# Kernel tuning notes

Measured on AMD Instinct MI355X. Metric: run time of the kernel, lower is better.

Reference implementation:

```python
import jax, jax.numpy as jnp
import numpy as np

V = 10000   # vocab_size
L = 12      # n_layer
H = 12      # n_head
C = 768     # n_embd
TE = 64     # t_embd
WTE = C - TE
BS = 1024   # block_size
B, T = 4, 1024
D = C // H
EPS = 1e-5


def setup_inputs() -> dict:
    key = jax.random.key(0)
    ks = jax.random.split(key, 12)
    s = 0.02
    def n(k, shape, extra=1.0):
        return jax.random.normal(k, shape, jnp.float32) * (s * extra)
    resid_scale = 1.0 / np.sqrt(2 * L)  # c_proj init std scaling from _init_weights loop
    return {
        'idx': jax.random.randint(ks[0], (B, T), 0, V),
        'ts': jax.random.uniform(ks[1], (B, T), jnp.float32) * 100.0,
        'wte': n(ks[2], (V, WTE)),
        'basis_freq': jnp.asarray(1.0 / 10 ** np.linspace(0, 9, TE), jnp.float32),
        'phase': jnp.zeros((TE,), jnp.float32),
        'wpe': n(ks[3], (BS, C)),
        'ln1_w': jnp.ones((L, C), jnp.float32), 'ln1_b': jnp.zeros((L, C), jnp.float32),
        'qkv_w': n(ks[4], (L, 3 * C, C)), 'qkv_b': jnp.zeros((L, 3 * C), jnp.float32),
        'proj_w': n(ks[5], (L, C, C), resid_scale), 'proj_b': jnp.zeros((L, C), jnp.float32),
        'ln2_w': jnp.ones((L, C), jnp.float32), 'ln2_b': jnp.zeros((L, C), jnp.float32),
        'fc_w': n(ks[6], (L, 4 * C, C)), 'fc_b': jnp.zeros((L, 4 * C), jnp.float32),
        'fc2_w': n(ks[7], (L, C, 4 * C), resid_scale), 'fc2_b': jnp.zeros((L, C), jnp.float32),
        'lnf_w': jnp.ones((C,), jnp.float32), 'lnf_b': jnp.zeros((C,), jnp.float32),
        'lm_w': n(ks[8], (V, C)),
        'tp_w': n(ks[9], (1, C)),
    }


def _ln(x, w, b):
    mu = jnp.mean(x, -1, keepdims=True)
    var = jnp.mean((x - mu) ** 2, -1, keepdims=True)
    return (x - mu) * jax.lax.rsqrt(var + EPS) * w + b


def reference(idx, ts, wte, basis_freq, phase, wpe, ln1_w, ln1_b, qkv_w, qkv_b,
              proj_w, proj_b, ln2_w, ln2_b, fc_w, fc_b, fc2_w, fc2_b,
              lnf_w, lnf_b, lm_w, tp_w):
    Bv, Tv = idx.shape
    tok = wte[idx]                                      # [B,T,C-TE]
    tim = jnp.cos(ts[..., None] * basis_freq + phase)   # TimeEncode -> [B,T,TE]
    x = jnp.concatenate([tok, tim], axis=-1) + wpe[:Tv]
    mask = jnp.tril(jnp.ones((Tv, Tv), bool))
    scale = 1.0 / np.sqrt(D)

    def block(x, p):
        l1w, l1b, qw, qb, pw, pb, l2w, l2b, fw, fb, f2w, f2b = p
        h = _ln(x, l1w, l1b)
        qkv = h @ qw.T + qb                              # [B,T,3C]
        q, k, v = jnp.split(qkv, 3, axis=-1)
        def heads(z):
            return z.reshape(Bv, Tv, H, D).transpose(0, 2, 1, 3)  # [B,H,T,D]
        q, k, v = heads(q), heads(k), heads(v)
        att = jnp.einsum('bhtd,bhsd->bhts', q, k) * scale
        att = jnp.where(mask, att, -jnp.inf)             # causal masked_fill
        att = jax.nn.softmax(att, axis=-1)
        y = jnp.einsum('bhts,bhsd->bhtd', att, v)
        y = y.transpose(0, 2, 1, 3).reshape(Bv, Tv, C)
        x = x + (y @ pw.T + pb)
        h2 = _ln(x, l2w, l2b)
        m = jax.nn.gelu(h2 @ fw.T + fb, approximate=False)  # torch nn.GELU default is exact
        x = x + (m @ f2w.T + f2b)
        return x, None

    x, _ = jax.lax.scan(block, x, (ln1_w, ln1_b, qkv_w, qkv_b, proj_w, proj_b,
                                   ln2_w, ln2_b, fc_w, fc_b, fc2_w, fc2_b))
    x = _ln(x, lnf_w, lnf_b)
    logits = x @ lm_w.T          # [B,T,V]
    tpred = x @ tp_w.T           # [B,T,1]
    return logits, tpred
```

## Files before the change

### kernel.cpp

```cpp
#include <hip/hip_runtime.h>
#include <hip/hip_bf16.h>
#include <math.h>

#define Bb   4
#define Tt   1024
#define Cc   768
#define Hh   12
#define Dd   64
#define Ll   12
#define Vv   10000
#define WTEe 704
#define MTOT 4096

#define QSCALE 0.18033688f

typedef __bf16 bf16x8 __attribute__((ext_vector_type(8)));
typedef float  f32x4  __attribute__((ext_vector_type(4)));
typedef unsigned short u16;

typedef const __attribute__((address_space(1))) void* gptr_t;
typedef __attribute__((address_space(3))) void* lptr_t;

__device__ inline void gload16(const void* g, void* l) {
    __builtin_amdgcn_global_load_lds((gptr_t)g, (lptr_t)l, 16, 0, 0);
}

__device__ inline u16 f2bf(float f) {
    unsigned int u = __float_as_uint(f);
    return (u16)((u + 0x7fffu + ((u >> 16) & 1u)) >> 16);
}
__device__ inline float bf2f(u16 u) { return __uint_as_float(((unsigned)u) << 16); }

__device__ inline float gelu_f(float v) {
    float t = v * (0.797884561f + 0.0356774081f * v * v);
    float e = __expf(2.f * t);
    float th = 1.f - 2.f / (e + 1.f);
    return 0.5f * v * (1.f + th);
}

#if __has_builtin(__builtin_amdgcn_exp2f)
__device__ inline float fast_exp2(float x) { return __builtin_amdgcn_exp2f(x); }
#else
__device__ inline float fast_exp2(float x) { return exp2f(x); }
#endif

#define WAITVM(N)  asm volatile("s_waitcnt vmcnt(" #N ")" ::: "memory")
#define WAITLGKM0() asm volatile("s_waitcnt lgkmcnt(0)" ::: "memory")
#define SCHEDB()   __builtin_amdgcn_sched_barrier(0)
#define SBAR()     __builtin_amdgcn_s_barrier()

__global__ __launch_bounds__(256)
void convert_pack(const float* __restrict__ in, u16* __restrict__ out,
                  int nk8, int K, int rowmod, int scaleLim)
{
    int i = blockIdx.x * 256 + threadIdx.x;
    if (i >= nk8) return;
    int row = (i << 3) / K;
    int col = (i << 3) % K;
    float s = 1.f;
    if (rowmod && (row % rowmod) < scaleLim) s = QSCALE;
    float4 v0 = ((const float4*)in)[2 * i];
    float4 v1 = ((const float4*)in)[2 * i + 1];
    uint4 o;
    o.x = (unsigned)f2bf(v0.x * s) | ((unsigned)f2bf(v0.y * s) << 16);
    o.y = (unsigned)f2bf(v0.z * s) | ((unsigned)f2bf(v0.w * s) << 16);
    o.z = (unsigned)f2bf(v1.x * s) | ((unsigned)f2bf(v1.y * s) << 16);
    o.w = (unsigned)f2bf(v1.z * s) | ((unsigned)f2bf(v1.w * s) << 16);
    int tile = row >> 4, kt = col >> 5;
    int l = (row & 15) | (((col >> 3) & 3) << 4);
    size_t off = (((size_t)tile * (K >> 5) + kt) << 9) + l * 8;
    *(uint4*)(out + off) = o;
}

__global__ __launch_bounds__(256)
void scale_qkvb(const float* __restrict__ in, float* __restrict__ out, int n)
{
    int i = blockIdx.x * 256 + threadIdx.x;
    if (i >= n) return;
    int col = i % (3 * Cc);
    out[i] = in[i] * (col < Cc ? QSCALE : 1.f);
}

__global__ __launch_bounds__(256)
void embed_kernel(const int* __restrict__ idx, const float* __restrict__ ts,
                  const float* __restrict__ wte, const float* __restrict__ freq,
                  const float* __restrict__ ph, const float* __restrict__ wpe,
                  float* __restrict__ x)
{
    const int bt  = blockIdx.x;
    const int t   = bt & (Tt - 1);
    const int tok = idx[bt];
    const float tv = ts[bt];
#pragma unroll
    for (int j = 0; j < 3; ++j) {
        int c = threadIdx.x + (j << 8);
        float val;
        if (c < WTEe) val = wte[(size_t)tok * WTEe + c];
        else {
            int e = c - WTEe;
            val = cosf(tv * freq[e] + ph[e]);
        }
        x[(size_t)bt * Cc + c] = val + wpe[(size_t)t * Cc + c];
    }
}

__global__ __launch_bounds__(256)
void ln_pack16(const float* __restrict__ x, const float* __restrict__ wt,
               const float* __restrict__ bs, u16* __restrict__ out)
{
    __shared__ float ps[256], ps2[256];
    const int tid  = threadIdx.x;
    const int tile = blockIdx.x;
    const int r0   = tile << 4;
    const int row  = tid & 15;
    const int g    = (tid >> 4) & 3;
    const int kt0  = tid >> 6;

    const float* xr = x + (size_t)(r0 + row) * Cc;
    float4 va[6], vb[6];
    float s = 0.f, s2 = 0.f;
#pragma unroll
    for (int it = 0; it < 6; ++it) {
        int col = (kt0 + 4 * it) * 32 + g * 8;
        va[it] = *(const float4*)(xr + col);
        vb[it] = *(const float4*)(xr + col + 4);
        s  += va[it].x + va[it].y + va[it].z + va[it].w
            + vb[it].x + vb[it].y + vb[it].z + vb[it].w;
        s2 += va[it].x * va[it].x + va[it].y * va[it].y
            + va[it].z * va[it].z + va[it].w * va[it].w
            + vb[it].x * vb[it].x + vb[it].y * vb[it].y
            + vb[it].z * vb[it].z + vb[it].w * vb[it].w;
    }
    ps[tid] = s;
    ps2[tid] = s2;
    __syncthreads();

    float st = 0.f, st2 = 0.f;
#pragma unroll
    for (int j = 0; j < 16; ++j) {
        st  += ps[row + 16 * j];
        st2 += ps2[row + 16 * j];
    }
    float mu = st * (1.f / 768.f);
    float var = st2 * (1.f / 768.f) - mu * mu;
    float rs = rsqrtf(var + 1e-5f);

    u16* ob = out + ((size_t)tile * 24 << 9);
    const int l = tid & 63;
#pragma unroll
    for (int it = 0; it < 6; ++it) {
        int kt  = kt0 + 4 * it;
        int col = kt * 32 + g * 8;
        ushort o[8];
        o[0] = f2bf((va[it].x - mu) * rs * wt[col]     + bs[col]);
        o[1] = f2bf((va[it].y - mu) * rs * wt[col + 1] + bs[col + 1]);
        o[2] = f2bf((va[it].z - mu) * rs * wt[col + 2] + bs[col + 2]);
        o[3] = f2bf((va[it].w - mu) * rs * wt[col + 3] + bs[col + 3]);
        o[4] = f2bf((vb[it].x - mu) * rs * wt[col + 4] + bs[col + 4]);
        o[5] = f2bf((vb[it].y - mu) * rs * wt[col + 5] + bs[col + 5]);
        o[6] = f2bf((vb[it].z - mu) * rs * wt[col + 6] + bs[col + 6]);
        o[7] = f2bf((vb[it].w - mu) * rs * wt[col + 7] + bs[col + 7]);
        *(uint4*)(ob + ((size_t)kt << 9) + l * 8) = *(uint4*)o;
    }
}

__device__ inline void st_out(float* p, size_t o, float v) { p[o] = v; }
__device__ inline void st_out(u16*   p, size_t o, float v) { p[o] = f2bf(v); }

template<int EPI, int APK, typename OutT>
__global__ __launch_bounds__(256)
void gemm_bf16(const u16* __restrict__ A, const u16* __restrict__ Wp,
               const float* __restrict__ bias, const float* __restrict__ resid,
               OutT* __restrict__ out, u16* __restrict__ vt, int N, int K)
{
    __shared__ uint4 AF[3][8][64];
    __shared__ uint4 BF[3][8][64];
    const int tid  = threadIdx.x;
    const int lane = tid & 63;
    const int w    = tid >> 6;
    const int wr   = w >> 1, wc = w & 1;
    const int lq   = lane & 15, g = lane >> 4;
    const int m0   = blockIdx.x * 128, n0 = blockIdx.y * 128;
    const int KB   = K >> 5;

    const u16 *ap0, *ap1;
    if (APK) {
        ap0 = A + ((((size_t)(m0 >> 4) + 2 * w) * KB) << 9) + lane * 8;
        ap1 = ap0 + ((size_t)KB << 9);
    } else {
        ap0 = A + (size_t)(m0 + (2 * w) * 16 + lq) * K + g * 8;
        ap1 = ap0 + (size_t)16 * K;
    }

    int tn0 = (n0 >> 4) + 2 * w, tn1 = tn0 + 1;
    const int tmax = (N >> 4) - 1;
    tn0 = tn0 < tmax ? tn0 : tmax;
    tn1 = tn1 < tmax ? tn1 : tmax;
    const u16* bq0 = Wp + (((size_t)tn0 * KB) << 9) + lane * 8;
    const u16* bq1 = Wp + (((size_t)tn1 * KB) << 9) + lane * 8;

    f32x4 acc[4][4] = {};
    const int nk = KB;

#define GSTAGE(s, sl) do {                                               \
        if (APK) {                                                       \
            gload16(ap0 + ((size_t)(s) << 9), &AF[sl][2 * w][lane]);     \
            gload16(ap1 + ((size_t)(s) << 9), &AF[sl][2 * w + 1][lane]); \
        } else {                                                         \
            gload16(ap0 + ((s) << 5), &AF[sl][2 * w][lane]);             \
            gload16(ap1 + ((s) << 5), &AF[sl][2 * w + 1][lane]);         \
        }                                                                \
        gload16(bq0 + ((size_t)(s) << 9), &BF[sl][2 * w][lane]);         \
        gload16(bq1 + ((size_t)(s) << 9), &BF[sl][2 * w + 1][lane]); } while (0)

    GSTAGE(0, 0);
    GSTAGE(1, 1);
    WAITVM(4);
    SCHEDB();
    SBAR();
    SCHEDB();

    int sl = 0;
    for (int t = 0; t < nk; ++t) {
        int sl2 = sl + 2; if (sl2 >= 3) sl2 -= 3;
        if (t + 2 < nk) GSTAGE(t + 2, sl2);

        bf16x8 af[4], bfr[4];
#pragma unroll
        for (int mi = 0; mi < 4; ++mi)
            af[mi] = __builtin_bit_cast(bf16x8, AF[sl][wr * 4 + mi][lane]);
#pragma unroll
        for (int ni = 0; ni < 4; ++ni)
            bfr[ni] = __builtin_bit_cast(bf16x8, BF[sl][wc * 4 + ni][lane]);
        __builtin_amdgcn_s_setprio(1);
#pragma unroll
        for (int mi = 0; mi < 4; ++mi)
#pragma unroll
            for (int ni = 0; ni < 4; ++ni)
                acc[mi][ni] = __builtin_amdgcn_mfma_f32_16x16x32_bf16(
                    af[mi], bfr[ni], acc[mi][ni], 0, 0, 0);
        __builtin_amdgcn_s_setprio(0);

        if (t + 2 < nk) { WAITVM(4); }
        else           { WAITVM(0); }
        SCHEDB();
        SBAR();
        SCHEDB();
        sl = (sl + 1 == 3) ? 0 : sl + 1;
    }
#undef GSTAGE

    if (EPI == 3 && n0 >= 1536) {
#pragma unroll
        for (int mi = 0; mi < 4; ++mi)
#pragma unroll
            for (int ni = 0; ni < 4; ++ni) {
                int col = n0 + wc * 64 + ni * 16 + lq;
                int c2  = col - 1536;
                int hh  = c2 >> 6, dd = c2 & 63;
                int row = m0 + wr * 64 + mi * 16 + g * 4;
                int bb  = row >> 10, tr = row & 1023;
                float bv = bias[col];
                ushort4 o;
                o.x = f2bf(acc[mi][ni][0] + bv);
                o.y = f2bf(acc[mi][ni][1] + bv);
                o.z = f2bf(acc[mi][ni][2] + bv);
                o.w = f2bf(acc[mi][ni][3] + bv);
                *(ushort4*)&vt[(((size_t)bb * Hh + hh) * Dd + dd) * Tt + tr] = o;
            }
        return;
    }

#pragma unroll
    for (int mi = 0; mi < 4; ++mi)
#pragma unroll
        for (int ni = 0; ni < 4; ++ni) {
            int col = n0 + wc * 64 + ni * 16 + lq;
            if (col >= N) continue;
            int row = m0 + wr * 64 + mi * 16 + g * 4;
            float bv = bias ? bias[col] : 0.f;
#pragma unroll
            for (int q = 0; q < 4; ++q) {
                float v = acc[mi][ni][q] + bv;
                size_t o = (size_t)(row + q) * N + col;
                if (EPI == 1) v += resid[o];
                if (EPI == 2) v = gelu_f(v);
                st_out(out, o, v);
            }
        }
}

__global__ __launch_bounds__(256)
void gemm_n64(const u16* __restrict__ A, const u16* __restrict__ Wp,
              const float* __restrict__ bias, const float* __restrict__ resid,
              float* __restrict__ out, int N, int K)
{
    __shared__ uint4 AF[2][8][64];
    __shared__ uint4 BF[2][16][64];
    const int tid  = threadIdx.x;
    const int lane = tid & 63;
    const int w    = tid >> 6;
    const int wr   = w & 1, wc = w >> 1;
    const int lq   = lane & 15, g = lane >> 4;
    const int m0   = blockIdx.x * 64, n0 = blockIdx.y * 128;
    const int KB   = K >> 5;
    const int nk   = K >> 6;

    const u16* ap = A + (size_t)(m0 + w * 16 + lq) * K + g * 8;
    int tn0 = (n0 >> 4) + 2 * w, tn1 = tn0 + 1;
    const int tmax = (N >> 4) - 1;
    tn0 = tn0 < tmax ? tn0 : tmax;
    tn1 = tn1 < tmax ? tn1 : tmax;
    const u16* bq0 = Wp + (((size_t)tn0 * KB) << 9) + lane * 8;
    const u16* bq1 = Wp + (((size_t)tn1 * KB) << 9) + lane * 8;

    f32x4 acc[2][4] = {};

#define GSTAGE(t, bi) do {                                                 \
        gload16(ap + ((t) << 6),      &AF[bi][2 * w][lane]);               \
        gload16(ap + ((t) << 6) + 32, &AF[bi][2 * w + 1][lane]);           \
        gload16(bq0 + ((size_t)(2 * (t)) << 9),     &BF[bi][4 * w][lane]); \
        gload16(bq0 + ((size_t)(2 * (t) + 1) << 9), &BF[bi][4 * w + 1][lane]); \
        gload16(bq1 + ((size_t)(2 * (t)) << 9),     &BF[bi][4 * w + 2][lane]); \
        gload16(bq1 + ((size_t)(2 * (t) + 1) << 9), &BF[bi][4 * w + 3][lane]); } while (0)

    GSTAGE(0, 0);
    WAITVM(0);
    SCHEDB();
    SBAR();
    SCHEDB();

    for (int t = 0; t < nk; ++t) {
        const int buf = t & 1;
        if (t + 1 < nk) GSTAGE(t + 1, buf ^ 1);

#pragma unroll
        for (int s = 0; s < 2; ++s) {
            bf16x8 a0 = __builtin_bit_cast(bf16x8, AF[buf][(wr * 2) * 2 + s][lane]);
            bf16x8 a1 = __builtin_bit_cast(bf16x8, AF[buf][(wr * 2 + 1) * 2 + s][lane]);
            bf16x8 bb[4];
#pragma unroll
            for (int ni = 0; ni < 4; ++ni)
                bb[ni] = __builtin_bit_cast(bf16x8, BF[buf][(wc * 4 + ni) * 2 + s][lane]);
            __builtin_amdgcn_s_setprio(1);
#pragma unroll
            for (int ni = 0; ni < 4; ++ni) {
                acc[0][ni] = __builtin_amdgcn_mfma_f32_16x16x32_bf16(
                    bb[ni], a0, acc[0][ni], 0, 0, 0);
                acc[1][ni] = __builtin_amdgcn_mfma_f32_16x16x32_bf16(
                    bb[ni], a1, acc[1][ni], 0, 0, 0);
            }
            __builtin_amdgcn_s_setprio(0);
        }

        WAITVM(0);
        SCHEDB();
        SBAR();
        SCHEDB();
    }
#undef GSTAGE

#pragma unroll
    for (int mi = 0; mi < 2; ++mi)
#pragma unroll
        for (int ni = 0; ni < 4; ++ni) {
            int m = m0 + (wr * 2 + mi) * 16 + lq;
            int n = n0 + wc * 64 + ni * 16 + (g << 2);
            float4 bv = *(const float4*)&bias[n];
            size_t o = (size_t)m * N + n;
            float4 rv = *(const float4*)&resid[o];
            float4 v;
            v.x = acc[mi][ni][0] + bv.x + rv.x;
            v.y = acc[mi][ni][1] + bv.y + rv.y;
            v.z = acc[mi][ni][2] + bv.z + rv.z;
            v.w = acc[mi][ni][3] + bv.w + rv.w;
            *(float4*)&out[o] = v;
        }
}

__global__ __launch_bounds__(512, 2)
void gemm8p(const u16* __restrict__ Apk, const u16* __restrict__ Wp,
            float* __restrict__ out, int N, int K)
{
    __shared__ uint4 AF[2][16][2][64];
    __shared__ uint4 BF[2][16][2][64];
    const int tid  = threadIdx.x;
    const int lane = tid & 63;
    const int w    = tid >> 6;
    const int wr   = w >> 2, wc = w & 3;
    const int lq   = lane & 15, g = lane >> 4;
    const int m0   = blockIdx.x * 256, n0 = blockIdx.y * 256;
    const int KB   = K >> 5;

    const u16* aq0 = Apk + ((((size_t)(m0 >> 4) + 2 * w) * KB) << 9) + lane * 8;
    const u16* aq1 = aq0 + ((size_t)KB << 9);

    int tn0 = (n0 >> 4) + 2 * w, tn1 = tn0 + 1;
    const int tmax = (N >> 4) - 1;
    tn0 = tn0 < tmax ? tn0 : tmax;
    tn1 = tn1 < tmax ? tn1 : tmax;
    const u16* bq0 = Wp + (((size_t)tn0 * KB) << 9) + lane * 8;
    const u16* bq1 = Wp + (((size_t)tn1 * KB) << 9) + lane * 8;

    f32x4 acc[8][4] = {};
    const int nt = K >> 6;

    gload16(aq0,       &AF[0][2 * w][0][lane]);
    gload16(aq1,       &AF[0][2 * w + 1][0][lane]);
    gload16(bq0,       &BF[0][2 * w][0][lane]);
    gload16(bq1,       &BF[0][2 * w + 1][0][lane]);
    gload16(aq0 + 512, &AF[0][2 * w][1][lane]);
    gload16(aq1 + 512, &AF[0][2 * w + 1][1][lane]);
    gload16(bq0 + 512, &BF[0][2 * w][1][lane]);
    gload16(bq1 + 512, &BF[0][2 * w + 1][1][lane]);
    WAITVM(0);
    SCHEDB();
    SBAR();

    int buf = 0;
    for (int t = 0; t < nt; ++t) {
        const bool more = (t + 1 < nt);
        const size_t bb0 = (size_t)(2 * (t + 1)) << 9;
        bf16x8 a0[4], a1[4], b0[4];

#pragma unroll
        for (int i = 0; i < 4; ++i)
            a0[i] = __builtin_bit_cast(bf16x8, AF[buf][wr * 8 + i][0][lane]);
#pragma unroll
        for (int i = 0; i < 4; ++i)
            b0[i] = __builtin_bit_cast(bf16x8, BF[buf][wc * 4 + i][0][lane]);
        if (more) {
            gload16(aq0 + bb0, &AF[buf ^ 1][2 * w][0][lane]);
            gload16(aq1 + bb0, &AF[buf ^ 1][2 * w + 1][0][lane]);
        }
        SCHEDB();
        SBAR();
        WAITLGKM0();
        SCHEDB();
        __builtin_amdgcn_s_setprio(1);
#pragma unroll
        for (int mi = 0; mi < 4; ++mi)
#pragma unroll
            for (int ni = 0; ni < 4; ++ni)
                acc[mi][ni] = __builtin_amdgcn_mfma_f32_16x16x32_bf16(
                    b0[ni], a0[mi], acc[mi][ni], 0, 0, 0);
        __builtin_amdgcn_s_setprio(0);
        SBAR();

#pragma unroll
        for (int i = 0; i < 4; ++i)
            a1[i] = __builtin_bit_cast(bf16x8, AF[buf][wr * 8 + 4 + i][0][lane]);
        if (more) {
            gload16(bq0 + bb0, &BF[buf ^ 1][2 * w][0][lane]);
            gload16(bq1 + bb0, &BF[buf ^ 1][2 * w + 1][0][lane]);
        }
        SCHEDB();
        SBAR();
        WAITLGKM0();
        SCHEDB();
        __builtin_amdgcn_s_setprio(1);
#pragma unroll
        for (int mi = 0; mi < 4; ++mi)
#pragma unroll
            for (int ni = 0; ni < 4; ++ni)
                acc[4 + mi][ni] = __builtin_amdgcn_mfma_f32_16x16x32_bf16(
                    b0[ni], a1[mi], acc[4 + mi][ni], 0, 0, 0);
        __builtin_amdgcn_s_setprio(0);
        if (more) { WAITVM(4); } else { WAITVM(0); }
        SCHEDB();
        SBAR();

#pragma unroll
        for (int i = 0; i < 4; ++i)
            a0[i] = __builtin_bit_cast(bf16x8, AF[buf][wr * 8 + i][1][lane]);
#pragma unroll
        for (int i = 0; i < 4; ++i)
            b0[i] = __builtin_bit_cast(bf16x8, BF[buf][wc * 4 + i][1][lane]);
        if (more) {
            gload16(aq0 + bb0 + 512, &AF[buf ^ 1][2 * w][1][lane]);
            gload16(aq1 + bb0 + 512, &AF[buf ^ 1][2 * w + 1][1][lane]);
        }
        SCHEDB();
        SBAR();
        WAITLGKM0();
        SCHEDB();
        __builtin_amdgcn_s_setprio(1);
#pragma unroll
        for (int mi = 0; mi < 4; ++mi)
#pragma unroll
            for (int ni = 0; ni < 4; ++ni)
                acc[mi][ni] = __builtin_amdgcn_mfma_f32_16x16x32_bf16(
                    b0[ni], a0[mi], acc[mi][ni], 0, 0, 0);
        __builtin_amdgcn_s_setprio(0);
        SBAR();

#pragma unroll
        for (int i = 0; i < 4; ++i)
            a1[i] = __builtin_bit_cast(bf16x8, AF[buf][wr * 8 + 4 + i][1][lane]);
        if (more) {
            gload16(bq0 + bb0 + 512, &BF[buf ^ 1][2 * w][1][lane]);
            gload16(bq1 + bb0 + 512, &BF[buf ^ 1][2 * w + 1][1][lane]);
        }
        SCHEDB();
        SBAR();
        WAITLGKM0();
        SCHEDB();
        __builtin_amdgcn_s_setprio(1);
#pragma unroll
        for (int mi = 0; mi < 4; ++mi)
#pragma unroll
            for (int ni = 0; ni < 4; ++ni)
                acc[4 + mi][ni] = __builtin_amdgcn_mfma_f32_16x16x32_bf16(
                    b0[ni], a1[mi], acc[4 + mi][ni], 0, 0, 0);
        __builtin_amdgcn_s_setprio(0);
        if (more) { WAITVM(4); } else { WAITVM(0); }
        SCHEDB();
        SBAR();

        buf ^= 1;
    }

#pragma unroll
    for (int mi = 0; mi < 8; ++mi)
#pragma unroll
        for (int ni = 0; ni < 4; ++ni) {
            int m = m0 + wr * 128 + mi * 16 + lq;
            int n = n0 + wc * 64 + ni * 16 + (g << 2);
            size_t o = (size_t)m * N + n;
            if (n + 3 < N) {
                float4 v;
                v.x = acc[mi][ni][0]; v.y = acc[mi][ni][1];
                v.z = acc[mi][ni][2]; v.w = acc[mi][ni][3];
                *(float4*)&out[o] = v;
            } else {
#pragma unroll
                for (int q = 0; q < 4; ++q)
                    if (n + q < N) out[o + q] = acc[mi][ni][q];
            }
        }
}

__global__ __launch_bounds__(512)
void attn_mfma(const u16* __restrict__ qkv, const u16* __restrict__ vt,
               u16* __restrict__ y)
{
    __shared__ uint4 KF[2][4][2][64];
    __shared__ uint4 VF[2][4][2][64];

    const int tid  = threadIdx.x;
    const int lane = tid & 63;
    const int w    = tid >> 6;
    const int lq   = lane & 15, g = lane >> 4;
    const int m    = gridDim.x - 1 - blockIdx.x;
    const int bh   = blockIdx.y;
    const int b    = bh / Hh, h = bh % Hh;
    const int wq0  = m * 128 + w * 16;
    const size_t base = (size_t)b * Tt * (3 * Cc);

    const u16* qrow = qkv + base + (size_t)(wq0 + lq) * (3 * Cc) + h * Dd;
    bf16x8 qf0 = __builtin_bit_cast(bf16x8, *(const uint4*)(qrow + g * 8));
    bf16x8 qf1 = __builtin_bit_cast(bf16x8, *(const uint4*)(qrow + 32 + g * 8));

    f32x4 yac[4] = {};
    float lrun = 0.f;

    const int wm = w & 3;
    const u16* kbase = qkv + base + Cc + h * Dd + (size_t)(wm * 16 + lq) * (3 * Cc) + g * 8;
    const u16* vbase = vt + ((size_t)bh * Dd + wm * 16 + lq) * Tt + g * 8;

#define STAGE(c, bi)  do {                                              \
        if (w < 4) {                                                    \
            const u16* kp = kbase + (size_t)(c) * 64 * (3 * Cc);        \
            gload16(kp,      &KF[bi][wm][0][lane]);                     \
            gload16(kp + 32, &KF[bi][wm][1][lane]);                     \
        } else {                                                        \
            const u16* vp = vbase + (c) * 64;                           \
            gload16(vp,      &VF[bi][wm][0][lane]);                     \
            gload16(vp + 32, &VF[bi][wm][1][lane]);                     \
        }                                                               \
    } while (0)

    const int nch = 2 * m + 2;
    STAGE(0, 0);
    WAITVM(0);
    SCHEDB();
    SBAR();

    const int srcb = lq + ((g & 1) << 5);

    int buf = 0;
    for (int c = 0; c < nch; ++c) {
        if (c + 1 < nch) STAGE(c + 1, buf ^ 1);

        f32x4 sc[4] = {};
        __builtin_amdgcn_s_setprio(1);
#pragma unroll
        for (int nt = 0; nt < 4; ++nt) {
            bf16x8 k0 = __builtin_bit_cast(bf16x8, KF[buf][nt][0][lane]);
            bf16x8 k1 = __builtin_bit_cast(bf16x8, KF[buf][nt][1][lane]);
            sc[nt] = __builtin_amdgcn_mfma_f32_16x16x32_bf16(k0, qf0, sc[nt], 0, 0, 0);
            sc[nt] = __builtin_amdgcn_mfma_f32_16x16x32_bf16(k1, qf1, sc[nt], 0, 0, 0);
        }
        __builtin_amdgcn_s_setprio(0);

        const int s0 = c * 64;
        if (s0 + 63 > wq0) {
            const int qg = wq0 + lq;
#pragma unroll
            for (int nt = 0; nt < 4; ++nt) {
                const int kb = s0 + nt * 16 + (g << 2);
#pragma unroll
                for (int j = 0; j < 4; ++j)
                    if (kb + j > qg) sc[nt][j] = -1e30f;
            }
        }

        float ls = 0.f;
#pragma unroll
        for (int nt = 0; nt < 4; ++nt)
#pragma unroll
            for (int j = 0; j < 4; ++j) {
                float p = fast_exp2(sc[nt][j]);
                sc[nt][j] = p;
                ls += p;
            }
        ls += __shfl_xor(ls, 16);
        ls += __shfl_xor(ls, 32);
        lrun += ls;

        unsigned pk[4][2];
#pragma unroll
        for (int nt = 0; nt < 4; ++nt) {
            unsigned u0 = __float_as_uint(sc[nt][0]);
            unsigned u1 = __float_as_uint(sc[nt][1]);
            unsigned u2 = __float_as_uint(sc[nt][2]);
            unsigned u3 = __float_as_uint(sc[nt][3]);
            pk[nt][0] = (u0 >> 16) | (u1 & 0xffff0000u);
            pk[nt][1] = (u2 >> 16) | (u3 & 0xffff0000u);
        }

        unsigned pa0[4], pa1[4];
#pragma unroll
        for (int m2 = 0; m2 < 4; ++m2) {
            int hsel = m2 & 1;
            int src  = srcb + ((m2 >> 1) << 4);
            unsigned lo0 = __shfl(pk[0][hsel], src);
            unsigned hi0 = __shfl(pk[1][hsel], src);
            unsigned lo1 = __shfl(pk[2][hsel], src);
            unsigned hi1 = __shfl(pk[3][hsel], src);
            pa0[m2] = (g >> 1) ? hi0 : lo0;
            pa1[m2] = (g >> 1) ? hi1 : lo1;
        }
        uint4 A0 = make_uint4(pa0[0], pa0[1], pa0[2], pa0[3]);
        uint4 A1 = make_uint4(pa1[0], pa1[1], pa1[2], pa1[3]);
        bf16x8 pA0 = __builtin_bit_cast(bf16x8, A0);
        bf16x8 pA1 = __builtin_bit_cast(bf16x8, A1);

        __builtin_amdgcn_s_setprio(1);
#pragma unroll
        for (int dt = 0; dt < 4; ++dt) {
            bf16x8 vb0 = __builtin_bit_cast(bf16x8, VF[buf][dt][0][lane]);
            bf16x8 vb1 = __builtin_bit_cast(bf16x8, VF[buf][dt][1][lane]);
            yac[dt] = __builtin_amdgcn_mfma_f32_16x16x32_bf16(pA0, vb0, yac[dt], 0, 0, 0);
            yac[dt] = __builtin_amdgcn_mfma_f32_16x16x32_bf16(pA1, vb1, yac[dt], 0, 0, 0);
        }
        __builtin_amdgcn_s_setprio(0);

        if (c + 1 < nch) { WAITVM(0); }
        SCHEDB();
        SBAR();
        buf ^= 1;
    }
#undef STAGE

    f32x4 rl;
#pragma unroll
    for (int j = 0; j < 4; ++j)
        rl[j] = 1.0f / __shfl(lrun, (g << 2) + j);
#pragma unroll
    for (int dt = 0; dt < 4; ++dt)
#pragma unroll
        for (int j = 0; j < 4; ++j)
            y[(size_t)(b * Tt + wq0 + (g << 2) + j) * Cc + h * Dd + dt * 16 + lq]
                = f2bf(yac[dt][j] * rl[j]);
}

__global__ __launch_bounds__(256)
void tpred_kernel(const u16* __restrict__ hp, const float* __restrict__ tp,
                  float* __restrict__ out)
{
    const int row  = blockIdx.x * 4 + (threadIdx.x >> 6);
    const int lane = threadIdx.x & 63;
    const int tile = row >> 4, r15 = row & 15;
    const u16* tb = hp + ((size_t)tile * 24 << 9);
    float s = 0.f;
#pragma unroll
    for (int j = 0; j < 12; ++j) {
        int col = lane + (j << 6);
        int kt = col >> 5, g = (col >> 3) & 3, e = col & 7;
        s += bf2f(tb[((size_t)kt << 9) + (r15 | (g << 4)) * 8 + e]) * tp[col];
    }
#pragma unroll
    for (int m = 32; m; m >>= 1) s += __shfl_xor(s, m);
    if (lane == 0) out[row] = s;
}

extern "C" void kernel_launch(void* const* d_in, const int* in_sizes, int n_in,
                              void* d_out, int out_size, void* d_ws, size_t ws_size,
                              hipStream_t stream)
{
    const int*   idx  = (const int*)d_in[0];
    const float* ts   = (const float*)d_in[1];
    const float* wte  = (const float*)d_in[2];
    const float* freq = (const float*)d_in[3];
    const float* ph   = (const float*)d_in[4];
    const float* wpe  = (const float*)d_in[5];
    const float* ln1w = (const float*)d_in[6];
    const float* ln1b = (const float*)d_in[7];
    const float* qkvw = (const float*)d_in[8];
    const float* qkvb = (const float*)d_in[9];
    const float* pw   = (const float*)d_in[10];
    const float* pb   = (const float*)d_in[11];
    const float* ln2w = (const float*)d_in[12];
    const float* ln2b = (const float*)d_in[13];
    const float* fcw  = (const float*)d_in[14];
    const float* fcb  = (const float*)d_in[15];
    const float* f2w  = (const float*)d_in[16];
    const float* f2b  = (const float*)d_in[17];
    const float* lnfw = (const float*)d_in[18];
    const float* lnfb = (const float*)d_in[19];
    const float* lmw  = (const float*)d_in[20];
    const float* tpw  = (const float*)d_in[21];
    float* out = (float*)d_out;

    const int n_qkvw = 3 * Cc * Cc, n_pw = Cc * Cc, n_fcw = 4 * Cc * Cc;

    char* p = (char*)d_ws;
    float* x    = (float*)p;               p += (size_t)MTOT * Cc * 4;
    u16*   qkvB = (u16*)p;                 p += (size_t)MTOT * 3 * Cc * 2;
    u16*   VtB  = (u16*)p;                 p += (size_t)Bb * Hh * Dd * Tt * 2;
    u16*   hB   = (u16*)p;                 p += (size_t)MTOT * Cc * 2;
    u16*   yB   = (u16*)p;                 p += (size_t)MTOT * Cc * 2;
    u16*   mbB  = (u16*)p;                 p += (size_t)MTOT * 4 * Cc * 2;
    u16*   lmwB = (u16*)p;                 p += (size_t)Vv * Cc * 2;
    float* sbias= (float*)p;               p += (size_t)Ll * 3 * Cc * 4;
    char* wbase = p;

    size_t need_big = (size_t)(wbase - (char*)d_ws)
                    + ((size_t)Ll * (n_qkvw + n_pw + 2 * n_fcw)) * 2;
    bool big = ws_size >= need_big;

    u16 *wqA, *wpA, *wfA, *wf2A;
    if (big) {
        wqA  = (u16*)wbase;                wbase += (size_t)Ll * n_qkvw * 2;
        wpA  = (u16*)wbase;                wbase += (size_t)Ll * n_pw * 2;
        wfA  = (u16*)wbase;                wbase += (size_t)Ll * n_fcw * 2;
        wf2A = (u16*)wbase;
    } else {
        wqA  = (u16*)wbase;                wbase += (size_t)n_qkvw * 2;
        wpA  = (u16*)wbase;                wbase += (size_t)n_pw * 2;
        wfA  = (u16*)wbase;                wbase += (size_t)n_fcw * 2;
        wf2A = (u16*)wbase;
    }

    auto pack = [&](const float* src, u16* dst, size_t rows, int K,
                    int rowmod, int scaleLim) {
        int nk8 = (int)(rows * K / 8);
        convert_pack<<<(nk8 + 255) / 256, 256, 0, stream>>>(
            src, dst, nk8, K, rowmod, scaleLim);
    };

    pack(lmw, lmwB, Vv, Cc, 0, 0);
    {
        int nb = Ll * 3 * Cc;
        scale_qkvb<<<(nb + 255) / 256, 256, 0, stream>>>(qkvb, sbias, nb);
    }
    if (big) {
        pack(qkvw, wqA,  (size_t)Ll * 3 * Cc, Cc, 3 * Cc, Cc);
        pack(pw,   wpA,  (size_t)Ll * Cc,     Cc, 0, 0);
        pack(fcw,  wfA,  (size_t)Ll * 4 * Cc, Cc, 0, 0);
        pack(f2w,  wf2A, (size_t)Ll * Cc, 4 * Cc, 0, 0);
    }
    embed_kernel<<<MTOT, 256, 0, stream>>>(idx, ts, wte, freq, ph, wpe, x);

    for (int l = 0; l < Ll; ++l) {
        u16 *wqB, *wpB, *wfB, *wf2B;
        if (big) {
            wqB  = wqA  + (size_t)l * n_qkvw;
            wpB  = wpA  + (size_t)l * n_pw;
            wfB  = wfA  + (size_t)l * n_fcw;
            wf2B = wf2A + (size_t)l * n_fcw;
        } else {
            wqB = wqA; wpB = wpA; wfB = wfA; wf2B = wf2A;
            pack(qkvw + (size_t)l * n_qkvw, wqB, 3 * Cc, Cc, 3 * Cc, Cc);
            pack(pw   + (size_t)l * n_pw,   wpB, Cc,     Cc, 0, 0);
            pack(fcw  + (size_t)l * n_fcw,  wfB, 4 * Cc, Cc, 0, 0);
            pack(f2w  + (size_t)l * n_fcw,  wf2B, Cc, 4 * Cc, 0, 0);
        }

        ln_pack16<<<MTOT / 16, 256, 0, stream>>>(x, ln1w + l * Cc, ln1b + l * Cc, hB);
        gemm_bf16<3, 1, u16><<<dim3(32, 18), 256, 0, stream>>>(
            hB, wqB, sbias + (size_t)l * 3 * Cc, nullptr, qkvB, VtB, 3 * Cc, Cc);
        attn_mfma<<<dim3(Tt / 128, Bb * Hh), 512, 0, stream>>>(qkvB, VtB, yB);
        gemm_n64<<<dim3(64, 6), 256, 0, stream>>>(
            yB, wpB, pb + (size_t)l * Cc, x, x, Cc, Cc);
        ln_pack16<<<MTOT / 16, 256, 0, stream>>>(x, ln2w + l * Cc, ln2b + l * Cc, hB);
        gemm_bf16<2, 1, u16><<<dim3(32, 24), 256, 0, stream>>>(
            hB, wfB, fcb + (size_t)l * 4 * Cc, nullptr, mbB, nullptr, 4 * Cc, Cc);
        gemm_n64<<<dim3(64, 6), 256, 0, stream>>>(
            mbB, wf2B, f2b + (size_t)l * Cc, x, x, Cc, 4 * Cc);
    }

    ln_pack16<<<MTOT / 16, 256, 0, stream>>>(x, lnfw, lnfb, hB);
    gemm8p<<<dim3(16, 40), 512, 0, stream>>>(hB, lmwB, out, Vv, Cc);
    tpred_kernel<<<MTOT / 4, 256, 0, stream>>>(hB, tpw, out + (size_t)MTOT * Vv);
}
```

Measured before the change: 2.432 ms.

## Emit FC GELU output in MFMA-packed tile layout for fc2 GEMM A loads

The FC GEMM's GELU epilogue now swaps the MFMA operands so each lane holds four consecutive output columns, and writes bf16 results straight into the 16x32 packed fragment layout. The fc2 GEMM gains a template flag that loads its A operand from that packed layout with contiguous 16-byte per-lane loads instead of strided row reads. This targets uncoalesced A-operand global loads in the K=3072 fc2 GEMM and produces vectorized stores in the FC epilogue. It couples the two kernels' layouts and depends on correct index math in the new store path.

```diff
diff --git a/kernel.cpp b/kernel.cpp
--- a/kernel.cpp
+++ b/kernel.cpp
@@ -236,9 +236,14 @@
 #pragma unroll
         for (int mi = 0; mi < 4; ++mi)
 #pragma unroll
-            for (int ni = 0; ni < 4; ++ni)
-                acc[mi][ni] = __builtin_amdgcn_mfma_f32_16x16x32_bf16(
-                    af[mi], bfr[ni], acc[mi][ni], 0, 0, 0);
+            for (int ni = 0; ni < 4; ++ni) {
+                if (EPI == 4)
+                    acc[mi][ni] = __builtin_amdgcn_mfma_f32_16x16x32_bf16(
+                        bfr[ni], af[mi], acc[mi][ni], 0, 0, 0);
+                else
+                    acc[mi][ni] = __builtin_amdgcn_mfma_f32_16x16x32_bf16(
+                        af[mi], bfr[ni], acc[mi][ni], 0, 0, 0);
+            }
         __builtin_amdgcn_s_setprio(0);
 
         if (t + 2 < nk) { WAITVM(4); }
@@ -249,6 +254,28 @@
         sl = (sl + 1 == 3) ? 0 : sl + 1;
     }
 #undef GSTAGE
+
+    if (EPI == 4) {
+        const int KB2 = N >> 5;
+#pragma unroll
+        for (int mi = 0; mi < 4; ++mi)
+#pragma unroll
+            for (int ni = 0; ni < 4; ++ni) {
+                int m = m0 + wr * 64 + mi * 16 + lq;
+                int n = n0 + wc * 64 + ni * 16 + (g << 2);
+                float4 bv = *(const float4*)&bias[n];
+                ushort4 o;
+                o.x = f2bf(gelu_f(acc[mi][ni][0] + bv.x));
+                o.y = f2bf(gelu_f(acc[mi][ni][1] + bv.y));
+                o.z = f2bf(gelu_f(acc[mi][ni][2] + bv.z));
+                o.w = f2bf(gelu_f(acc[mi][ni][3] + bv.w));
+                int tile = m >> 4, kt = n >> 5;
+                int l2 = (m & 15) | (((n >> 3) & 3) << 4);
+                *(ushort4*)&((u16*)out)[(((size_t)tile * KB2 + kt) << 9)
+                                        + l2 * 8 + (n & 7)] = o;
+            }
+        return;
+    }
 
     if (EPI == 3 && n0 >= 1536) {
 #pragma unroll
@@ -290,6 +317,7 @@
         }
 }
 
+template<int APK>
 __global__ __launch_bounds__(256)
 void gemm_n64(const u16* __restrict__ A, const u16* __restrict__ Wp,
               const float* __restrict__ bias, const float* __restrict__ resid,
@@ -306,7 +334,10 @@
     const int KB   = K >> 5;
     const int nk   = K >> 6;
 
-    const u16* ap = A + (size_t)(m0 + w * 16 + lq) * K + g * 8;
+    const u16* ap;
+    if (APK) ap = A + ((((size_t)(m0 >> 4) + w) * KB) << 9) + lane * 8;
+    else     ap = A + (size_t)(m0 + w * 16 + lq) * K + g * 8;
+
     int tn0 = (n0 >> 4) + 2 * w, tn1 = tn0 + 1;
     const int tmax = (N >> 4) - 1;
     tn0 = tn0 < tmax ? tn0 : tmax;
@@ -317,8 +348,13 @@
     f32x4 acc[2][4] = {};
 
 #define GSTAGE(t, bi) do {                                                 \
-        gload16(ap + ((t) << 6),      &AF[bi][2 * w][lane]);               \
-        gload16(ap + ((t) << 6) + 32, &AF[bi][2 * w + 1][lane]);           \
+        if (APK) {                                                         \
+            gload16(ap + ((size_t)(2 * (t)) << 9),     &AF[bi][2 * w][lane]);     \
+            gload16(ap + ((size_t)(2 * (t) + 1) << 9), &AF[bi][2 * w + 1][lane]); \
+        } else {                                                           \
+            gload16(ap + ((t) << 6),      &AF[bi][2 * w][lane]);           \
+            gload16(ap + ((t) << 6) + 32, &AF[bi][2 * w + 1][lane]);       \
+        }                                                                  \
         gload16(bq0 + ((size_t)(2 * (t)) << 9),     &BF[bi][4 * w][lane]); \
         gload16(bq0 + ((size_t)(2 * (t) + 1) << 9), &BF[bi][4 * w + 1][lane]); \
         gload16(bq1 + ((size_t)(2 * (t)) << 9),     &BF[bi][4 * w + 2][lane]); \
@@ -802,12 +838,12 @@
         gemm_bf16<3, 1, u16><<<dim3(32, 18), 256, 0, stream>>>(
             hB, wqB, sbias + (size_t)l * 3 * Cc, nullptr, qkvB, VtB, 3 * Cc, Cc);
         attn_mfma<<<dim3(Tt / 128, Bb * Hh), 512, 0, stream>>>(qkvB, VtB, yB);
-        gemm_n64<<<dim3(64, 6), 256, 0, stream>>>(
+        gemm_n64<0><<<dim3(64, 6), 256, 0, stream>>>(
             yB, wpB, pb + (size_t)l * Cc, x, x, Cc, Cc);
         ln_pack16<<<MTOT / 16, 256, 0, stream>>>(x, ln2w + l * Cc, ln2b + l * Cc, hB);
-        gemm_bf16<2, 1, u16><<<dim3(32, 24), 256, 0, stream>>>(
+        gemm_bf16<4, 1, u16><<<dim3(32, 24), 256, 0, stream>>>(
             hB, wfB, fcb + (size_t)l * 4 * Cc, nullptr, mbB, nullptr, 4 * Cc, Cc);
-        gemm_n64<<<dim3(64, 6), 256, 0, stream>>>(
+        gemm_n64<1><<<dim3(64, 6), 256, 0, stream>>>(
             mbB, wf2B, f2b + (size_t)l * Cc, x, x, Cc, 4 * Cc);
     }
 
```

New measurement: 2.563 ms. 5.3% more time.
